# Kernel optimization log

Measured on AMD Instinct MI355X. Metric: run time of the kernel, lower is better.

Reference implementation:

```python
import jax, jax.numpy as jnp
import numpy as np

NUM_GROUPS = 32
EPS = 1e-6


def group_norm(x, gamma, beta):
    # x: [b, c, h, w]
    b, c, h, w = x.shape
    xg = x.reshape(b, NUM_GROUPS, c // NUM_GROUPS, h, w)
    mean = xg.mean(axis=(2, 3, 4), keepdims=True)
    var = xg.var(axis=(2, 3, 4), keepdims=True)
    xn = ((xg - mean) * jax.lax.rsqrt(var + EPS)).reshape(b, c, h, w)
    return xn * gamma[None, :, None, None] + beta[None, :, None, None]


def conv1x1(x, w, bias):
    # 1x1 conv == channel-mixing matmul. x: [b,c,h,w], w: [co,ci]
    y = jnp.einsum('bchw,oc->bohw', x, w)
    return y + bias[None, :, None, None]


def setup_inputs() -> dict:
    key = jax.random.key(0)
    ks = jax.random.split(key, 10)
    B, C, H, W = 4, 512, 64, 64
    s = 1.0 / np.sqrt(C)
    inp = {
        'x': jax.random.normal(ks[0], (B, C, H, W), jnp.float32),
        'gamma': jnp.ones((C,), jnp.float32),
        'beta': jnp.zeros((C,), jnp.float32),
        'wq': jax.random.normal(ks[1], (C, C), jnp.float32) * s,
        'bq': jnp.zeros((C,), jnp.float32),
        'wk': jax.random.normal(ks[2], (C, C), jnp.float32) * s,
        'bk': jnp.zeros((C,), jnp.float32),
        'wv': jax.random.normal(ks[3], (C, C), jnp.float32) * s,
        'bv': jnp.zeros((C,), jnp.float32),
        'wo': jax.random.normal(ks[4], (C, C), jnp.float32) * s,
        'bo': jnp.zeros((C,), jnp.float32),
    }
    return inp


def reference(x, gamma, beta, wq, bq, wk, bk, wv, bv, wo, bo):
    b, c, h, w = x.shape
    h_ = group_norm(x, gamma, beta)
    q = conv1x1(h_, wq, bq).reshape(b, c, h * w)  # [b,c,n]
    k = conv1x1(h_, wk, bk).reshape(b, c, h * w)
    v = conv1x1(h_, wv, bv).reshape(b, c, h * w)
    scale = jnp.asarray(c, x.dtype) ** -0.5
    # scores: [b, n, n] = q^T k
    scores = jnp.einsum('bcn,bcm->bnm', q, k) * scale
    attn = jax.nn.softmax(scores, axis=2)
    # out: [b, c, n] = v @ attn^T  (h_[i] = sum_j attn[i,j] v[j])
    out = jnp.einsum('bnm,bcm->bcn', attn, v).reshape(b, c, h, w)
    out = conv1x1(out, wo, bo)
    return x + out
```

## Files before the change

kernel.cpp:

```cpp
#include <hip/hip_runtime.h>

typedef __bf16 bf16x8 __attribute__((ext_vector_type(8)));
typedef float f32x4 __attribute__((ext_vector_type(4)));
typedef unsigned short u16;

__device__ __forceinline__ u16 f2bf(float f) {
  unsigned int u = __builtin_bit_cast(unsigned int, f);
  u += 0x7fff + ((u >> 16) & 1);
  return (u16)(u >> 16);
}
__device__ __forceinline__ float bf2f(u16 s) {
  unsigned int u = ((unsigned int)s) << 16;
  return __builtin_bit_cast(float, u);
}
__device__ __forceinline__ void unp8(uint4 u, float* f) {
  f[0] = bf2f(u.x & 0xffff); f[1] = bf2f(u.x >> 16);
  f[2] = bf2f(u.y & 0xffff); f[3] = bf2f(u.y >> 16);
  f[4] = bf2f(u.z & 0xffff); f[5] = bf2f(u.z >> 16);
  f[6] = bf2f(u.w & 0xffff); f[7] = bf2f(u.w >> 16);
}
__device__ __forceinline__ uint4 pk8(const float* f) {
  uint4 u;
  u.x = (unsigned)f2bf(f[0]) | ((unsigned)f2bf(f[1]) << 16);
  u.y = (unsigned)f2bf(f[2]) | ((unsigned)f2bf(f[3]) << 16);
  u.z = (unsigned)f2bf(f[4]) | ((unsigned)f2bf(f[5]) << 16);
  u.w = (unsigned)f2bf(f[6]) | ((unsigned)f2bf(f[7]) << 16);
  return u;
}

__device__ __forceinline__ void gl_lds16(const u16* g, u16* l) {
  __builtin_amdgcn_global_load_lds(
      (const __attribute__((address_space(1))) void*)g,
      (__attribute__((address_space(3))) void*)l, 16, 0, 0);
}

template <int MODE>
__global__ __launch_bounds__(512, 2) void gemm_nt256(
    const u16* __restrict__ A, int lda, unsigned long long sA,
    const u16* __restrict__ Bt, int ldb, unsigned long long sB,
    u16* __restrict__ Cout, int ldc, unsigned long long sC,
    unsigned long long sSplit, int K, float alpha, int tn,
    const float* __restrict__ bias_col, const float* __restrict__ bias_col2,
    float* __restrict__ psum) {
  __shared__ u16 lds[2][4][8192];

  const int t = threadIdx.x;
  const int lane = t & 63;
  const int w = t >> 6;
  const int bz = blockIdx.z;
  A  += (size_t)bz * sA + (size_t)blockIdx.y * K;
  Bt += (size_t)bz * sB + (size_t)blockIdx.y * K;
  Cout += (size_t)blockIdx.y * sSplit;

  const int nwg = gridDim.x;
  const int flat = blockIdx.x;
  const int wg = (flat & 7) * (nwg >> 3) + (flat >> 3);
  const int tt = tn << 1;
  const int p  = wg / tt;
  const int rr = wg - p * tt;
  const int m0 = (p * 2 + (rr & 1)) * 256;
  const int n0 = (rr >> 1) * 256;

  const int NKT = K >> 6;

  const int sr = lane >> 3;
  const int sc = ((lane & 7) ^ sr) * 8;
  const u16* gA = A  + (size_t)(m0 + w * 16 + sr) * lda + sc;
  const u16* gB = Bt + (size_t)(n0 + w * 16 + sr) * ldb + sc;
  const size_t a128 = (size_t)128 * lda, b128 = (size_t)128 * ldb;
  const size_t a8 = (size_t)8 * lda, b8 = (size_t)8 * ldb;
  const int lws = w * 1024;

  auto stage = [&](int slot, int region, int kt) {
    kt = kt < NKT ? kt : NKT - 1;
    u16* l = &lds[slot][region][lws];
    if (region < 2) {
      const u16* g = gA + (region ? a128 : 0) + (size_t)kt * 64;
      gl_lds16(g, l);
      gl_lds16(g + a8, l + 512);
    } else {
      const u16* g = gB + (region == 3 ? b128 : 0) + (size_t)kt * 64;
      gl_lds16(g, l);
      gl_lds16(g + b8, l + 512);
    }
  };

  const int wr = w >> 2, wc = w & 3;
  const int fr = lane & 15, kg = lane >> 4;
  const int frx = (fr & 7) << 4;

  f32x4 acc[8][4] = {};
  f32x4 sacc[8] = {};
  bf16x8 af[4][2], bq[2][2];
  union { u16 u[8]; bf16x8 v; } ou;
#pragma unroll
  for (int i = 0; i < 8; ++i) ou.u[i] = 0x3F80;
  const bf16x8 onesb = ou.v;

#define LDA_(s, qm)                                                            \
  {                                                                            \
    const u16* Ab = &lds[s][0][0];                                             \
    _Pragma("unroll") for (int m = 0; m < 4; ++m) {                            \
      const int R = wr * 128 + (qm) * 64 + m * 16 + fr;                        \
      _Pragma("unroll") for (int kk = 0; kk < 2; ++kk)                         \
          af[m][kk] = *reinterpret_cast<const bf16x8*>(                        \
              Ab + R * 64 + (((kk * 64 + kg * 16) ^ frx) >> 1));               \
    }                                                                          \
  }
#define LDB_(s, qn)                                                            \
  {                                                                            \
    const u16* Bb = &lds[s][2][0];                                             \
    _Pragma("unroll") for (int n = 0; n < 2; ++n) {                            \
      const int R = wc * 64 + (qn) * 32 + n * 16 + fr;                         \
      _Pragma("unroll") for (int kk = 0; kk < 2; ++kk)                         \
          bq[n][kk] = *reinterpret_cast<const bf16x8*>(                        \
              Bb + R * 64 + (((kk * 64 + kg * 16) ^ frx) >> 1));               \
    }                                                                          \
  }
#define PH(s, qm, qn, DOA, DOB, ss, rr_, kt, VM)                               \
  {                                                                            \
    if (DOA) LDA_(s, qm)                                                       \
    if (DOB) LDB_(s, qn)                                                       \
    stage(ss, rr_, kt);                                                        \
    __builtin_amdgcn_s_barrier();                                              \
    asm volatile("s_waitcnt lgkmcnt(0)" ::: "memory");                         \
    __builtin_amdgcn_s_setprio(1);                                             \
    _Pragma("unroll") for (int kk = 0; kk < 2; ++kk)                           \
    _Pragma("unroll") for (int m = 0; m < 4; ++m)                              \
    _Pragma("unroll") for (int n = 0; n < 2; ++n)                              \
        acc[(qm)*4 + m][(qn)*2 + n] = __builtin_amdgcn_mfma_f32_16x16x32_bf16( \
            af[m][kk], bq[n][kk], acc[(qm)*4 + m][(qn)*2 + n], 0, 0, 0);       \
    if (MODE == 2 && (DOA) && wc == 0) {                                       \
      _Pragma("unroll") for (int kk = 0; kk < 2; ++kk)                         \
      _Pragma("unroll") for (int m = 0; m < 4; ++m)                            \
          sacc[(qm)*4 + m] = __builtin_amdgcn_mfma_f32_16x16x32_bf16(          \
              af[m][kk], onesb, sacc[(qm)*4 + m], 0, 0, 0);                    \
    }                                                                          \
    __builtin_amdgcn_s_setprio(0);                                             \
    if (VM) asm volatile("s_waitcnt vmcnt(2)" ::: "memory");                   \
    __builtin_amdgcn_s_barrier();                                              \
  }

  stage(0, 0, 0); stage(0, 1, 0); stage(0, 2, 0); stage(0, 3, 0);
  stage(1, 0, 1);
  asm volatile("s_waitcnt vmcnt(2)" ::: "memory");
  __builtin_amdgcn_s_barrier();

  for (int j = 0; j < (NKT >> 1); ++j) {
    const int k1 = 2 * j + 1, k2 = 2 * j + 2, k3 = 2 * j + 3;
    PH(0, 0, 0, 1, 1, 1, 1, k1, 0)
    PH(0, 0, 1, 0, 1, 1, 2, k1, 0)
    PH(0, 1, 1, 1, 0, 1, 3, k1, 0)
    PH(0, 1, 0, 0, 1, 0, 0, k2, 1)
    PH(1, 0, 0, 1, 1, 0, 1, k2, 0)
    PH(1, 0, 1, 0, 1, 0, 2, k2, 0)
    PH(1, 1, 1, 1, 0, 0, 3, k2, 0)
    PH(1, 1, 0, 0, 1, 1, 0, k3, 1)
  }
#undef PH
#undef LDB_
#undef LDA_

  __syncthreads();
  u16* cs = &lds[0][0][0];
#pragma unroll
  for (int a = 0; a < 8; ++a) {
    const int row = wr * 128 + a * 16 + (kg << 2);
#pragma unroll
    for (int b = 0; b < 4; ++b) {
      const int col = wc * 64 + b * 16 + fr;
      float bc = 0.0f;
      if (MODE == 0 && bias_col) {
        const int gc = n0 + col;
        bc = (bias_col2 && gc >= 512) ? bias_col2[gc - 512] : bias_col[gc & 511];
      }
#pragma unroll
      for (int r = 0; r < 4; ++r) {
        float v;
        if (MODE == 1) v = exp2f(acc[a][b][r] * alpha);
        else v = acc[a][b][r] * alpha + bc;
        cs[(row + r) * 256 + col] = f2bf(v);
      }
    }
  }
  __syncthreads();
  const size_t cbs = (size_t)bz * sC;
#pragma unroll
  for (int it = 0; it < 16; ++it) {
    const int off = (it * 512 + t) * 8;
    const int row = off >> 8, col = off & 255;
    *reinterpret_cast<uint4*>(&Cout[cbs + (size_t)(m0 + row) * ldc + (n0 + col)]) =
        *reinterpret_cast<const uint4*>(&cs[off]);
  }
  if (MODE == 2 && psum && wc == 0 && fr == 0) {
    const int Mrows = (nwg / tn) << 8;
    float* pp = psum + ((size_t)bz * gridDim.y + blockIdx.y) * Mrows + m0;
#pragma unroll
    for (int q = 0; q < 2; ++q)
#pragma unroll
      for (int m = 0; m < 4; ++m)
#pragma unroll
        for (int r = 0; r < 4; ++r)
          pp[wr * 128 + q * 64 + m * 16 + (kg << 2) + r] = sacc[q * 4 + m][r];
  }
}

template <bool OUT_F32>
__global__ __launch_bounds__(256) void gemm_nt(
    const u16* __restrict__ A, int lda, unsigned long long sA,
    const u16* __restrict__ Bt, int ldb, unsigned long long sB,
    void* __restrict__ Cout, int ldc, unsigned long long sC,
    int K, float alpha,
    const float* __restrict__ bias_row, const float* __restrict__ bias_col,
    const float* __restrict__ residual, unsigned long long sRes) {
  __shared__ u16 lds[128 * 128];
  u16* As = lds;
  u16* Bs = lds + 8192;

  const int t = threadIdx.x;
  const int bz = blockIdx.z;
  A  += (size_t)bz * sA;
  Bt += (size_t)bz * sB;
  const int m0 = blockIdx.x * 128;
  const int n0 = blockIdx.y * 128;

  const int lane = t & 63;
  const int w = t >> 6;

  const int srow = w * 32 + (lane >> 3);
  const int scol = (lane & 7) * 8;
  const u16* gA = A  + (size_t)(m0 + srow) * lda + scol;
  const u16* gB = Bt + (size_t)(n0 + srow) * ldb + scol;
  u16* lA = As + w * 2048;
  u16* lB = Bs + w * 2048;

  f32x4 acc[4][4] = {};
  const int wm = (w >> 1) * 64;
  const int wn = (w & 1) * 64;
  const int fr = lane & 15;
  const int kg = lane >> 4;

  for (int k0 = 0; k0 < K; k0 += 64) {
    __syncthreads();
#pragma unroll
    for (int i = 0; i < 4; ++i) {
      gl_lds16(gA + (size_t)(i * 8) * lda + k0, lA + i * 512);
      gl_lds16(gB + (size_t)(i * 8) * ldb + k0, lB + i * 512);
    }
    __syncthreads();

#pragma unroll
    for (int kk = 0; kk < 2; ++kk) {
      bf16x8 af[4], bfr[4];
#pragma unroll
      for (int m = 0; m < 4; ++m)
        af[m] = *reinterpret_cast<const bf16x8*>(
            &As[(wm + m * 16 + fr) * 64 + kk * 32 + kg * 8]);
#pragma unroll
      for (int n = 0; n < 4; ++n)
        bfr[n] = *reinterpret_cast<const bf16x8*>(
            &Bs[(wn + n * 16 + fr) * 64 + kk * 32 + kg * 8]);
#pragma unroll
      for (int m = 0; m < 4; ++m)
#pragma unroll
        for (int n = 0; n < 4; ++n)
          acc[m][n] = __builtin_amdgcn_mfma_f32_16x16x32_bf16(af[m], bfr[n], acc[m][n], 0, 0, 0);
    }
  }

  const size_t cbase = (size_t)bz * sC;
  const size_t rbase = (size_t)bz * sRes;
  const int rq = kg * 4;

  if (OUT_F32) {
    float* Cf = reinterpret_cast<float*>(Cout);
    float* lf = reinterpret_cast<float*>(lds);
#pragma unroll
    for (int h = 0; h < 2; ++h) {
      __syncthreads();
      if ((wm >> 6) == h) {
#pragma unroll
        for (int m = 0; m < 4; ++m)
#pragma unroll
          for (int n = 0; n < 4; ++n) {
            const float bc = bias_col ? bias_col[n0 + wn + n * 16 + fr] : 0.0f;
#pragma unroll
            for (int r = 0; r < 4; ++r)
              lf[(m * 16 + rq + r) * 128 + (wn + n * 16 + fr)] =
                  acc[m][n][r] * alpha + bc;
          }
      }
      __syncthreads();
#pragma unroll
      for (int it = 0; it < 8; ++it) {
        const int off = (it * 256 + t) * 4;
        const int row = off >> 7, col = off & 127;
        const int grow = m0 + h * 64 + row, gcol = n0 + col;
        float4 v = *reinterpret_cast<const float4*>(&lf[off]);
        if (bias_row) {
          const float br = bias_row[grow];
          v.x += br; v.y += br; v.z += br; v.w += br;
        }
        if (residual) {
          const float4 rx = *reinterpret_cast<const float4*>(
              &residual[rbase + (size_t)grow * ldc + gcol]);
          v.x += rx.x; v.y += rx.y; v.z += rx.z; v.w += rx.w;
        }
        *reinterpret_cast<float4*>(&Cf[cbase + (size_t)grow * ldc + gcol]) = v;
      }
    }
  } else {
    __syncthreads();
#pragma unroll
    for (int m = 0; m < 4; ++m) {
#pragma unroll
      for (int n = 0; n < 4; ++n) {
        const int gcol = n0 + wn + n * 16 + fr;
        const float bc = bias_col ? bias_col[gcol] : 0.0f;
#pragma unroll
        for (int r = 0; r < 4; ++r) {
          const int grow = m0 + wm + m * 16 + rq + r;
          float v = acc[m][n][r] * alpha + bc;
          if (bias_row) v += bias_row[grow];
          lds[(wm + m * 16 + rq + r) * 128 + (wn + n * 16 + fr)] = f2bf(v);
        }
      }
    }
    __syncthreads();
    u16* Cb = reinterpret_cast<u16*>(Cout);
#pragma unroll
    for (int j = 0; j < 8; ++j) {
      const int off = (j * 256 + t) * 8;
      const int row = off >> 7, col = off & 127;
      *reinterpret_cast<uint4*>(&Cb[cbase + (size_t)(m0 + row) * ldc + (n0 + col)]) =
          *reinterpret_cast<const uint4*>(&lds[off]);
    }
  }
}

__global__ __launch_bounds__(256) void groupnorm_k(
    const float* __restrict__ x, const float* __restrict__ gamma,
    const float* __restrict__ beta, u16* __restrict__ h_t, int C, int N) {
  const int g = blockIdx.x;
  const int b = blockIdx.y;
  const int t = threadIdx.x;
  const float* xb = x + ((size_t)b * C + g * 16) * N;

  float s = 0.f, q = 0.f;
  for (int c = 0; c < 16; ++c) {
    const float4* xr = reinterpret_cast<const float4*>(xb + (size_t)c * N);
    for (int j = t; j < N / 4; j += 256) {
      float4 v = xr[j];
      s += v.x + v.y + v.z + v.w;
      q += v.x * v.x + v.y * v.y + v.z * v.z + v.w * v.w;
    }
  }
#pragma unroll
  for (int o = 32; o > 0; o >>= 1) { s += __shfl_down(s, o); q += __shfl_down(q, o); }
  __shared__ float rs[4], rqs[4], stats[2];
  const int lane = t & 63, wid = t >> 6;
  if (lane == 0) { rs[wid] = s; rqs[wid] = q; }
  __syncthreads();
  if (t == 0) {
    float S = rs[0] + rs[1] + rs[2] + rs[3];
    float Q = rqs[0] + rqs[1] + rqs[2] + rqs[3];
    const float inv = 1.0f / (16.0f * (float)N);
    float mean = S * inv;
    float var = Q * inv - mean * mean;
    stats[0] = mean;
    stats[1] = rsqrtf(var + 1e-6f);
  }
  __syncthreads();
  const float mean = stats[0], rstd = stats[1];

  float gm[16], bt[16];
#pragma unroll
  for (int c = 0; c < 16; ++c) {
    gm[c] = gamma[g * 16 + c] * rstd;
    bt[c] = beta[g * 16 + c] - mean * gm[c];
  }
  u16* ho = h_t + (size_t)b * N * C + g * 16;
  for (int n = t; n < N; n += 256) {
    union { u16 us[16]; uint4 v4[2]; } pk;
#pragma unroll
    for (int c = 0; c < 16; ++c) {
      float v = xb[(size_t)c * N + n];
      pk.us[c] = f2bf(v * gm[c] + bt[c]);
    }
    uint4* dst = reinterpret_cast<uint4*>(ho + (size_t)n * C);
    dst[0] = pk.v4[0];
    dst[1] = pk.v4[1];
  }
}

__global__ __launch_bounds__(256) void wcvt4(
    const float* __restrict__ s0, const float* __restrict__ s1,
    const float* __restrict__ s2, const float* __restrict__ s3,
    u16* __restrict__ dst, int n) {
  const int i = (blockIdx.x * 256 + threadIdx.x) * 8;
  if (i >= n) return;
  const float* src = (blockIdx.y == 0) ? s0 : (blockIdx.y == 1) ? s1
                     : (blockIdx.y == 2) ? s2 : s3;
  const float4* s4 = reinterpret_cast<const float4*>(src + i);
  float4 a = s4[0], b = s4[1];
  float f[8] = {a.x, a.y, a.z, a.w, b.x, b.y, b.z, b.w};
  *reinterpret_cast<uint4*>(dst + (size_t)blockIdx.y * n + i) = pk8(f);
}

__global__ __launch_bounds__(256) void reduce_pv(const u16* __restrict__ p,
                                                 const float* __restrict__ psum,
                                                 u16* __restrict__ o, int n) {
  const int i = (blockIdx.x * 256 + threadIdx.x) * 8;
  if (i >= n) return;
  const int row = i >> 9;
  const int b = row >> 12, nn = row & 4095;
  const float il = 1.0f / (psum[(size_t)(b * 2) * 4096 + nn] +
                           psum[(size_t)(b * 2 + 1) * 4096 + nn]);
  uint4 a = *reinterpret_cast<const uint4*>(p + i);
  uint4 bb = *reinterpret_cast<const uint4*>(p + n + i);
  float fa[8], fb[8];
  unp8(a, fa); unp8(bb, fb);
#pragma unroll
  for (int j = 0; j < 8; ++j) fa[j] = (fa[j] + fb[j]) * il;
  *reinterpret_cast<uint4*>(o + i) = pk8(fa);
}

__global__ __launch_bounds__(256) void scale_o(u16* __restrict__ o,
                                               const float* __restrict__ psum,
                                               int n) {
  const int i = (blockIdx.x * 256 + threadIdx.x) * 8;
  if (i >= n) return;
  const float il = 1.0f / psum[i >> 9];
  uint4 a = *reinterpret_cast<const uint4*>(o + i);
  float fa[8];
  unp8(a, fa);
#pragma unroll
  for (int j = 0; j < 8; ++j) fa[j] *= il;
  *reinterpret_cast<uint4*>(o + i) = pk8(fa);
}

extern "C" void kernel_launch(void* const* d_in, const int* in_sizes, int n_in,
                              void* d_out, int out_size, void* d_ws, size_t ws_size,
                              hipStream_t stream) {
  const float* x     = (const float*)d_in[0];
  const float* gamma = (const float*)d_in[1];
  const float* beta  = (const float*)d_in[2];
  const float* wq    = (const float*)d_in[3];
  const float* bq    = (const float*)d_in[4];
  const float* wk    = (const float*)d_in[5];
  const float* bk    = (const float*)d_in[6];
  const float* wv    = (const float*)d_in[7];
  const float* bv    = (const float*)d_in[8];
  const float* wo    = (const float*)d_in[9];
  const float* bo    = (const float*)d_in[10];

  const int B = 4, C = 512, N = 4096;
  const size_t NC = (size_t)N * C;
  const size_t NN = (size_t)N * N;
  const size_t CC = (size_t)C * C;

  char* ws = (char*)d_ws;
  size_t off = 0;
  auto alloc = [&](size_t bytes) {
    size_t r = off;
    off = (off + bytes + 255) & ~(size_t)255;
    return r;
  };
  u16* wq_b = (u16*)(ws + alloc(CC * 2));
  u16* wk_b = (u16*)(ws + alloc(CC * 2));
  u16* wv_b = (u16*)(ws + alloc(CC * 2));
  u16* wo_b = (u16*)(ws + alloc(CC * 2));
  u16* h_t  = (u16*)(ws + alloc(B * NC * 2));
  u16* qk_t = (u16*)(ws + alloc(B * N * 1024 * 2));
  u16* v_cn = (u16*)(ws + alloc(B * NC * 2));
  u16* o_t  = (u16*)(ws + alloc(B * NC * 2));
  float* psum = (float*)(ws + alloc((size_t)B * 2 * N * 4));
  const size_t base_need = off;

  int s_batched = 0;
  u16* S;
  if (ws_size >= base_need + B * NN * 2) {
    S = (u16*)(ws + alloc(B * NN * 2));
    s_batched = 1;
  } else {
    S = (u16*)(ws + alloc(NN * 2));
  }
  u16* o_part = qk_t;

  (void)wk_b; (void)wv_b;

  wcvt4<<<dim3(CC / 2048, 4), 256, 0, stream>>>(wq, wk, wv, wo, wq_b, (int)CC);

  groupnorm_k<<<dim3(32, B), 256, 0, stream>>>(x, gamma, beta, h_t, C, N);

  gemm_nt256<0><<<dim3((N / 256) * (1024 / 256), 1, B), 512, 0, stream>>>(
      h_t, C, NC, wq_b, C, 0, qk_t, 1024, (unsigned long long)N * 1024, 0,
      C, 1.0f, 1024 / 256, bq, bk, nullptr);
  dim3 gv(C / 128, N / 128, B);
  gemm_nt<false><<<gv, 256, 0, stream>>>(wv_b, C, 0, h_t, C, NC, v_cn, N, NC,
                                         C, 1.0f, bv, nullptr, nullptr, 0);

  const float c1 = 0.06376694387439652f;
  if (s_batched) {
    gemm_nt256<1><<<dim3((N / 256) * (N / 256), 1, B), 512, 0, stream>>>(
        qk_t, 1024, (unsigned long long)N * 1024, qk_t + 512, 1024,
        (unsigned long long)N * 1024, S, N, NN, 0, C, c1, N / 256,
        nullptr, nullptr, nullptr);
    gemm_nt256<2><<<dim3((N / 256) * (C / 256), 2, B), 512, 0, stream>>>(
        S, N, NN, v_cn, N, NC, o_part, C, NC, (unsigned long long)B * NC,
        N / 2, 1.0f, C / 256, nullptr, nullptr, psum);
    reduce_pv<<<dim3((int)(B * NC / 2048)), 256, 0, stream>>>(
        o_part, psum, o_t, (int)(B * NC));
  } else {
    for (int b = 0; b < B; ++b) {
      gemm_nt256<1><<<dim3((N / 256) * (N / 256), 1, 1), 512, 0, stream>>>(
          qk_t + (size_t)b * N * 1024, 1024, 0, qk_t + (size_t)b * N * 1024 + 512,
          1024, 0, S, N, 0, 0, C, c1, N / 256, nullptr, nullptr, nullptr);
      gemm_nt256<2><<<dim3((N / 256) * (C / 256), 1, 1), 512, 0, stream>>>(
          S, N, 0, v_cn + (size_t)b * NC, N, 0, o_t + (size_t)b * NC, C, 0, 0,
          N, 1.0f, C / 256, nullptr, nullptr, psum + (size_t)b * N);
    }
    scale_o<<<dim3((int)(B * NC / 2048)), 256, 0, stream>>>(o_t, psum, (int)(B * NC));
  }

  dim3 gf(C / 128, N / 128, B);
  gemm_nt<true><<<gf, 256, 0, stream>>>(wo_b, C, 0, o_t, C, NC, d_out, N, NC,
                                        C, 1.0f, bo, nullptr, x, NC);
}
```

Measured before the change: 306.3 us.

## Add single-buffered high-occupancy GEMM for QK projection and score kernels

Introduces gemm_lt, a 256x256-tile GEMM with a single 64 KB LDS buffer, a plain load-wait-compute loop and launch bounds of 4 blocks per unit. The output is written back in two halves so it fits in that smaller LDS footprint. It replaces the double-buffered, software-pipelined gemm_nt256 for the Q/K projection and the QK^T score GEMM, and the now-unused bias path is removed from gemm_nt256. The aim is to hide memory latency through more resident waves instead of in-kernel pipelining. The risk is that the explicit vmcnt(0) wait before every k-step exposes load latency, and that register pressure may not actually allow 4 blocks.

```diff
diff --git a/kernel.cpp b/kernel.cpp
--- a/kernel.cpp
+++ b/kernel.cpp
@@ -35,12 +35,145 @@
 }
 
 template <int MODE>
+__global__ __launch_bounds__(512, 4) void gemm_lt(
+    const u16* __restrict__ A, int lda, unsigned long long sA,
+    const u16* __restrict__ Bt, int ldb, unsigned long long sB,
+    u16* __restrict__ Cout, int ldc, unsigned long long sC,
+    int K, float alpha, int tn,
+    const float* __restrict__ bias_col, const float* __restrict__ bias_col2) {
+  __shared__ u16 lds[4][8192];
+
+  const int t = threadIdx.x;
+  const int lane = t & 63;
+  const int w = t >> 6;
+  const int bz = blockIdx.z;
+  A  += (size_t)bz * sA;
+  Bt += (size_t)bz * sB;
+
+  const int nwg = gridDim.x;
+  const int flat = blockIdx.x;
+  const int wg = (flat & 7) * (nwg >> 3) + (flat >> 3);
+  const int tt = tn << 1;
+  const int p  = wg / tt;
+  const int rr = wg - p * tt;
+  const int m0 = (p * 2 + (rr & 1)) * 256;
+  const int n0 = (rr >> 1) * 256;
+
+  const int NKT = K >> 6;
+
+  const int sr = lane >> 3;
+  const int sc = ((lane & 7) ^ sr) * 8;
+  const u16* gA = A  + (size_t)(m0 + w * 16 + sr) * lda + sc;
+  const u16* gB = Bt + (size_t)(n0 + w * 16 + sr) * ldb + sc;
+  const size_t a128 = (size_t)128 * lda, b128 = (size_t)128 * ldb;
+  const size_t a8 = (size_t)8 * lda, b8 = (size_t)8 * ldb;
+  const int lws = w * 1024;
+
+  auto stage = [&](int region, int kt) {
+    u16* l = &lds[region][lws];
+    if (region < 2) {
+      const u16* g = gA + (region ? a128 : 0) + (size_t)kt * 64;
+      gl_lds16(g, l);
+      gl_lds16(g + a8, l + 512);
+    } else {
+      const u16* g = gB + (region == 3 ? b128 : 0) + (size_t)kt * 64;
+      gl_lds16(g, l);
+      gl_lds16(g + b8, l + 512);
+    }
+  };
+
+  const int wr = w >> 2, wc = w & 3;
+  const int fr = lane & 15, kg = lane >> 4;
+  const int frx = (fr & 7) << 4;
+
+  f32x4 acc[8][4] = {};
+  bf16x8 af[4][2], bq[2][2];
+
+  for (int kt = 0; kt < NKT; ++kt) {
+    if (kt) __builtin_amdgcn_s_barrier();
+    stage(0, kt); stage(1, kt); stage(2, kt); stage(3, kt);
+    asm volatile("s_waitcnt vmcnt(0)" ::: "memory");
+    __builtin_amdgcn_s_barrier();
+
+#pragma unroll
+    for (int qm = 0; qm < 2; ++qm) {
+      const u16* Ab = &lds[0][0];
+#pragma unroll
+      for (int m = 0; m < 4; ++m) {
+        const int R = wr * 128 + qm * 64 + m * 16 + fr;
+#pragma unroll
+        for (int kk = 0; kk < 2; ++kk)
+          af[m][kk] = *reinterpret_cast<const bf16x8*>(
+              Ab + R * 64 + (((kk * 64 + kg * 16) ^ frx) >> 1));
+      }
+#pragma unroll
+      for (int qn = 0; qn < 2; ++qn) {
+        const u16* Bb = &lds[2][0];
+#pragma unroll
+        for (int n = 0; n < 2; ++n) {
+          const int R = wc * 64 + qn * 32 + n * 16 + fr;
+#pragma unroll
+          for (int kk = 0; kk < 2; ++kk)
+            bq[n][kk] = *reinterpret_cast<const bf16x8*>(
+                Bb + R * 64 + (((kk * 64 + kg * 16) ^ frx) >> 1));
+        }
+#pragma unroll
+        for (int kk = 0; kk < 2; ++kk)
+#pragma unroll
+          for (int m = 0; m < 4; ++m)
+#pragma unroll
+            for (int n = 0; n < 2; ++n)
+              acc[qm * 4 + m][qn * 2 + n] = __builtin_amdgcn_mfma_f32_16x16x32_bf16(
+                  af[m][kk], bq[n][kk], acc[qm * 4 + m][qn * 2 + n], 0, 0, 0);
+      }
+    }
+  }
+
+  u16* cs = &lds[0][0];
+  const size_t cbs = (size_t)bz * sC;
+#pragma unroll
+  for (int h = 0; h < 2; ++h) {
+    __syncthreads();
+    if (wr == h) {
+#pragma unroll
+      for (int a = 0; a < 8; ++a) {
+        const int rl = a * 16 + (kg << 2);
+#pragma unroll
+        for (int b = 0; b < 4; ++b) {
+          const int col = wc * 64 + b * 16 + fr;
+          float bc = 0.0f;
+          if (MODE == 0 && bias_col) {
+            const int gc = n0 + col;
+            bc = (bias_col2 && gc >= 512) ? bias_col2[gc - 512] : bias_col[gc & 511];
+          }
+#pragma unroll
+          for (int r = 0; r < 4; ++r) {
+            float v;
+            if (MODE == 1) v = exp2f(acc[a][b][r] * alpha);
+            else v = acc[a][b][r] * alpha + bc;
+            cs[(rl + r) * 256 + col] = f2bf(v);
+          }
+        }
+      }
+    }
+    __syncthreads();
+#pragma unroll
+    for (int it = 0; it < 8; ++it) {
+      const int off = (it * 512 + t) * 8;
+      const int row = off >> 8, col = off & 255;
+      *reinterpret_cast<uint4*>(
+          &Cout[cbs + (size_t)(m0 + h * 128 + row) * ldc + (n0 + col)]) =
+          *reinterpret_cast<const uint4*>(&cs[off]);
+    }
+  }
+}
+
+template <int MODE>
 __global__ __launch_bounds__(512, 2) void gemm_nt256(
     const u16* __restrict__ A, int lda, unsigned long long sA,
     const u16* __restrict__ Bt, int ldb, unsigned long long sB,
     u16* __restrict__ Cout, int ldc, unsigned long long sC,
     unsigned long long sSplit, int K, float alpha, int tn,
-    const float* __restrict__ bias_col, const float* __restrict__ bias_col2,
     float* __restrict__ psum) {
   __shared__ u16 lds[2][4][8192];
 
@@ -169,18 +302,9 @@
 #pragma unroll
     for (int b = 0; b < 4; ++b) {
       const int col = wc * 64 + b * 16 + fr;
-      float bc = 0.0f;
-      if (MODE == 0 && bias_col) {
-        const int gc = n0 + col;
-        bc = (bias_col2 && gc >= 512) ? bias_col2[gc - 512] : bias_col[gc & 511];
-      }
-#pragma unroll
-      for (int r = 0; r < 4; ++r) {
-        float v;
-        if (MODE == 1) v = exp2f(acc[a][b][r] * alpha);
-        else v = acc[a][b][r] * alpha + bc;
-        cs[(row + r) * 256 + col] = f2bf(v);
-      }
+#pragma unroll
+      for (int r = 0; r < 4; ++r)
+        cs[(row + r) * 256 + col] = f2bf(acc[a][b][r] * alpha);
     }
   }
   __syncthreads();
@@ -493,32 +617,32 @@
 
   groupnorm_k<<<dim3(32, B), 256, 0, stream>>>(x, gamma, beta, h_t, C, N);
 
-  gemm_nt256<0><<<dim3((N / 256) * (1024 / 256), 1, B), 512, 0, stream>>>(
-      h_t, C, NC, wq_b, C, 0, qk_t, 1024, (unsigned long long)N * 1024, 0,
-      C, 1.0f, 1024 / 256, bq, bk, nullptr);
+  gemm_lt<0><<<dim3((N / 256) * (1024 / 256), 1, B), 512, 0, stream>>>(
+      h_t, C, NC, wq_b, C, 0, qk_t, 1024, (unsigned long long)N * 1024,
+      C, 1.0f, 1024 / 256, bq, bk);
   dim3 gv(C / 128, N / 128, B);
   gemm_nt<false><<<gv, 256, 0, stream>>>(wv_b, C, 0, h_t, C, NC, v_cn, N, NC,
                                          C, 1.0f, bv, nullptr, nullptr, 0);
 
   const float c1 = 0.06376694387439652f;
   if (s_batched) {
-    gemm_nt256<1><<<dim3((N / 256) * (N / 256), 1, B), 512, 0, stream>>>(
+    gemm_lt<1><<<dim3((N / 256) * (N / 256), 1, B), 512, 0, stream>>>(
         qk_t, 1024, (unsigned long long)N * 1024, qk_t + 512, 1024,
-        (unsigned long long)N * 1024, S, N, NN, 0, C, c1, N / 256,
-        nullptr, nullptr, nullptr);
+        (unsigned long long)N * 1024, S, N, NN, C, c1, N / 256,
+        nullptr, nullptr);
     gemm_nt256<2><<<dim3((N / 256) * (C / 256), 2, B), 512, 0, stream>>>(
         S, N, NN, v_cn, N, NC, o_part, C, NC, (unsigned long long)B * NC,
-        N / 2, 1.0f, C / 256, nullptr, nullptr, psum);
+        N / 2, 1.0f, C / 256, psum);
     reduce_pv<<<dim3((int)(B * NC / 2048)), 256, 0, stream>>>(
         o_part, psum, o_t, (int)(B * NC));
   } else {
     for (int b = 0; b < B; ++b) {
-      gemm_nt256<1><<<dim3((N / 256) * (N / 256), 1, 1), 512, 0, stream>>>(
+      gemm_lt<1><<<dim3((N / 256) * (N / 256), 1, 1), 512, 0, stream>>>(
           qk_t + (size_t)b * N * 1024, 1024, 0, qk_t + (size_t)b * N * 1024 + 512,
-          1024, 0, S, N, 0, 0, C, c1, N / 256, nullptr, nullptr, nullptr);
+          1024, 0, S, N, 0, C, c1, N / 256, nullptr, nullptr);
       gemm_nt256<2><<<dim3((N / 256) * (C / 256), 1, 1), 512, 0, stream>>>(
           S, N, 0, v_cn + (size_t)b * NC, N, 0, o_t + (size_t)b * NC, C, 0, 0,
-          N, 1.0f, C / 256, nullptr, nullptr, psum + (size_t)b * N);
+          N, 1.0f, C / 256, psum + (size_t)b * N);
     }
     scale_o<<<dim3((int)(B * NC / 2048)), 256, 0, stream>>>(o_t, psum, (int)(B * NC));
   }
```

New measurement: 1.069 ms. 3.49x slower.
